# Kernel optimization log

Hardware: AMD Instinct MI355X
Metric: run time of the kernel (lower is better)

## Reference

```python
import jax, jax.numpy as jnp
import numpy as np

B, INF, OUTF, SEQ, FUT = 128, 64, 16, 512, 96
H, L = 512, 2
PROJ = INF - OUTF  # proj_size = 48 (PyTorch LSTM proj_size semantics)


def _cell(x, h, c, Wih, Whh, bih, bhh, Whr):
    # One LSTM-with-projection step; PyTorch gate order: i, f, g, o
    gates = x @ Wih.T + h @ Whh.T + bih + bhh  # (B, 4H)
    i, f, g, o = jnp.split(gates, 4, axis=-1)
    c = jax.nn.sigmoid(f) * c + jax.nn.sigmoid(i) * jnp.tanh(g)
    h = (jax.nn.sigmoid(o) * jnp.tanh(c)) @ Whr.T  # projected hidden (B, PROJ)
    return h, c


def _run_layer(xs, p):
    # xs: (T, B, F) time-major; returns (T, B, PROJ), final (h, c)
    Wih, Whh, bih, bhh, Whr = p
    bsz = xs.shape[1]
    h0 = jnp.zeros((bsz, PROJ), xs.dtype)
    c0 = jnp.zeros((bsz, H), xs.dtype)
    def step(carry, x_t):
        h, c = carry
        h, c = _cell(x_t, h, c, Wih, Whh, bih, bhh, Whr)
        return (h, c), h
    (hT, cT), hs = jax.lax.scan(step, (h0, c0), xs)
    return hs, hT, cT


def _encoder(x_btf, layers):
    xs = jnp.swapaxes(x_btf, 0, 1)  # (T, B, INF)
    hTs, cTs = [], []
    for p in layers:
        xs, hT, cT = _run_layer(xs, p)
        hTs.append(hT); cTs.append(cT)
    return jnp.swapaxes(xs, 0, 1), tuple(hTs), tuple(cTs)


def _decoder(h0s, c0s, first_prev, dec_btf, layers):
    xs = jnp.swapaxes(dec_btf, 0, 1)  # (FUT, B, OUTF)
    def step(carry, x_t):
        hs, cs, prev = carry
        inp = jnp.concatenate([prev, x_t], axis=-1)  # (B, INF)
        nh, nc = [], []
        for l, p in enumerate(layers):
            h, c = _cell(inp, hs[l], cs[l], *p)
            nh.append(h); nc.append(c)
            inp = h
        return (tuple(nh), tuple(nc), inp), inp
    _, preds = jax.lax.scan(step, (h0s, c0s, first_prev), xs)
    return jnp.swapaxes(preds, 0, 1)  # (B, FUT, PROJ)


def _forward(theta, insample_x_t, outsample_x_t, enc_layers, dec_layers):
    x = jnp.transpose(insample_x_t, (0, 2, 1))      # (B, SEQ, INF)
    dec = jnp.transpose(outsample_x_t, (0, 2, 1))   # (B, FUT, OUTF)
    backcast_seq, hTs, cTs = _encoder(x, enc_layers)  # (B, SEQ, PROJ)
    first_prev = x[:, -1, :PROJ]  # input_elements[:, -1, :-OUTF]
    preds = _decoder(hTs, cTs, first_prev, dec, dec_layers)  # (B, FUT, PROJ)
    backcast_basis = jnp.transpose(backcast_seq, (0, 2, 1))  # (B, PROJ, SEQ)
    forecast_basis = jnp.transpose(preds, (0, 2, 1))         # (B, PROJ, FUT)
    cut = forecast_basis.shape[1]
    backcast = jnp.einsum('bp,bpt->bt', theta[:, cut:], backcast_basis)
    forecast = jnp.einsum('bp,bpt->bt', theta[:, :cut], forecast_basis)
    return backcast, forecast


def setup_inputs() -> dict:
    key = jax.random.key(0)
    ks = iter(jax.random.split(key, 64))
    s = 1.0 / float(np.sqrt(H))
    def u(shape):
        return jax.random.uniform(next(ks), shape, jnp.float32, -s, s)
    inp = {
        "theta": jax.random.normal(next(ks), (B, 2 * PROJ), jnp.float32),
        "insample_x_t": jax.random.normal(next(ks), (B, INF, SEQ), jnp.float32),
        "outsample_x_t": jax.random.normal(next(ks), (B, OUTF, FUT), jnp.float32),
    }
    for net in ("enc", "dec"):
        for l in range(L):
            in_dim = INF if l == 0 else PROJ
            inp[f"{net}_Wih{l}"] = u((4 * H, in_dim))
            inp[f"{net}_Whh{l}"] = u((4 * H, PROJ))
            inp[f"{net}_bih{l}"] = u((4 * H,))
            inp[f"{net}_bhh{l}"] = u((4 * H,))
            inp[f"{net}_Whr{l}"] = u((PROJ, H))
    return inp


def reference(theta, insample_x_t, outsample_x_t,
              enc_Wih0, enc_Whh0, enc_bih0, enc_bhh0, enc_Whr0,
              enc_Wih1, enc_Whh1, enc_bih1, enc_bhh1, enc_Whr1,
              dec_Wih0, dec_Whh0, dec_bih0, dec_bhh0, dec_Whr0,
              dec_Wih1, dec_Whh1, dec_bih1, dec_bhh1, dec_Whr1):
    enc_layers = [(enc_Wih0, enc_Whh0, enc_bih0, enc_bhh0, enc_Whr0),
                  (enc_Wih1, enc_Whh1, enc_bih1, enc_bhh1, enc_Whr1)]
    dec_layers = [(dec_Wih0, dec_Whh0, dec_bih0, dec_bhh0, dec_Whr0),
                  (dec_Wih1, dec_Whh1, dec_bih1, dec_bhh1, dec_Whr1)]
    return _forward(theta, insample_x_t, outsample_x_t, enc_layers, dec_layers)
```

## Files before the change

kernel.cpp:

```cpp
#include <hip/hip_runtime.h>
#include <cstdint>
#include <cstddef>

#define BATCH 128
#define INF   64
#define OUTF  16
#define SEQ   512
#define FUT   96
#define HID   512
#define G4    2048
#define PROJ  48
#define ECH   4

#define DRG 8
#define DBG 8
#define DUP 64
#define DBP 16

typedef float f32x4 __attribute__((ext_vector_type(4)));

__device__ __forceinline__ float fsigmoid(float x) {
    float e = __builtin_amdgcn_exp2f(-1.4426950408889634f * x);
    return __builtin_amdgcn_rcpf(1.0f + e);
}
__device__ __forceinline__ float ftanh(float x) {
    float e = __builtin_amdgcn_exp2f(2.8853900817779268f * x);
    return 1.0f - 2.0f * __builtin_amdgcn_rcpf(1.0f + e);
}

__device__ __forceinline__ float gload(const float* p) {
    return __hip_atomic_load(p, __ATOMIC_RELAXED, __HIP_MEMORY_SCOPE_AGENT);
}
__device__ __forceinline__ void gstore(float* p, float v) {
    __hip_atomic_store(p, v, __ATOMIC_RELAXED, __HIP_MEMORY_SCOPE_AGENT);
}

__device__ __forceinline__ f32x4 gsum8(const float* p, size_t stride) {
    f32x4 a0, a1, a2, a3, a4, a5, a6, a7;
    asm volatile(
        "global_load_dwordx4 %0, %8, off sc0 sc1\n\t"
        "global_load_dwordx4 %1, %9, off sc0 sc1\n\t"
        "global_load_dwordx4 %2, %10, off sc0 sc1\n\t"
        "global_load_dwordx4 %3, %11, off sc0 sc1\n\t"
        "global_load_dwordx4 %4, %12, off sc0 sc1\n\t"
        "global_load_dwordx4 %5, %13, off sc0 sc1\n\t"
        "global_load_dwordx4 %6, %14, off sc0 sc1\n\t"
        "global_load_dwordx4 %7, %15, off sc0 sc1\n\t"
        "s_waitcnt vmcnt(0)"
        : "=&v"(a0), "=&v"(a1), "=&v"(a2), "=&v"(a3),
          "=&v"(a4), "=&v"(a5), "=&v"(a6), "=&v"(a7)
        : "v"(p), "v"(p + stride), "v"(p + 2 * stride), "v"(p + 3 * stride),
          "v"(p + 4 * stride), "v"(p + 5 * stride), "v"(p + 6 * stride),
          "v"(p + 7 * stride)
        : "memory");
    return ((a0 + a1) + (a2 + a3)) + ((a4 + a5) + (a6 + a7));
}

__device__ __forceinline__ void bsync(unsigned* ctr, unsigned target, int tid) {
    asm volatile("s_waitcnt vmcnt(0)" ::: "memory");
    __syncthreads();
    if (tid == 0) {
        __hip_atomic_fetch_add(ctr, 1u, __ATOMIC_RELAXED, __HIP_MEMORY_SCOPE_AGENT);
        while (__hip_atomic_load(ctr, __ATOMIC_RELAXED, __HIP_MEMORY_SCOPE_AGENT) < target)
            __builtin_amdgcn_s_sleep(2);
    }
    __syncthreads();
    asm volatile("" ::: "memory");
}

__global__ void k_wtrans(const float* __restrict__ W, float* __restrict__ WT,
                         int R, int C) {
    __shared__ float tile[32][33];
    int r0 = blockIdx.x * 32, c0 = blockIdx.y * 32;
    int tx = threadIdx.x, ty = threadIdx.y;
    #pragma unroll
    for (int i = 0; i < 4; ++i) {
        int r = r0 + ty + 8 * i;
        if (r < R && c0 + tx < C) tile[ty + 8 * i][tx] = W[(size_t)r * C + c0 + tx];
    }
    __syncthreads();
    #pragma unroll
    for (int i = 0; i < 4; ++i) {
        int c = c0 + ty + 8 * i;
        if (c < C && r0 + tx < R) WT[(size_t)c * R + r0 + tx] = tile[tx][ty + 8 * i];
    }
}

__global__ __launch_bounds__(512) void k_enc(
    const float* __restrict__ x,
    const float* __restrict__ WT0, const float* __restrict__ Whh0,
    const float* __restrict__ bih0, const float* __restrict__ bhh0,
    const float* __restrict__ Whr0,
    const float* __restrict__ WT1, const float* __restrict__ Whh1,
    const float* __restrict__ bih1, const float* __restrict__ bhh1,
    const float* __restrict__ Whr1,
    float* __restrict__ H0x, float* __restrict__ H1,
    float* __restrict__ hs, float* __restrict__ cs,
    unsigned* __restrict__ eflags)
{
    const bool L1w = blockIdx.x >= BATCH;
    const int b = L1w ? blockIdx.x - BATCH : blockIdx.x;
    const int j = threadIdx.x;
    const int wave = j >> 6, lane = j & 63;
    const float* WT  = L1w ? WT1 : WT0;
    const float* Whh = L1w ? Whh1 : Whh0;
    const float* Whr = L1w ? Whr1 : Whr0;
    const float* bih = L1w ? bih1 : bih0;
    const float* bhh = L1w ? bhh1 : bhh0;
    const int K = L1w ? PROJ : INF;

    __shared__ float whr[PROJ][HID + 4];
    __shared__ __align__(16) float xs[ECH][INF + 4];
    __shared__ __align__(16) float ht_lds[HID];
    __shared__ __align__(16) float h_cur[PROJ];

    float wI[PROJ], wF[PROJ], wG[PROJ], wO[PROJ];
    #pragma unroll
    for (int k4 = 0; k4 < 12; ++k4) {
        float4 vi = *reinterpret_cast<const float4*>(&Whh[(size_t)j * PROJ + 4 * k4]);
        float4 vf = *reinterpret_cast<const float4*>(&Whh[(size_t)(j + HID) * PROJ + 4 * k4]);
        float4 vg = *reinterpret_cast<const float4*>(&Whh[(size_t)(j + 2 * HID) * PROJ + 4 * k4]);
        float4 vo = *reinterpret_cast<const float4*>(&Whh[(size_t)(j + 3 * HID) * PROJ + 4 * k4]);
        wI[4*k4+0]=vi.x; wI[4*k4+1]=vi.y; wI[4*k4+2]=vi.z; wI[4*k4+3]=vi.w;
        wF[4*k4+0]=vf.x; wF[4*k4+1]=vf.y; wF[4*k4+2]=vf.z; wF[4*k4+3]=vf.w;
        wG[4*k4+0]=vg.x; wG[4*k4+1]=vg.y; wG[4*k4+2]=vg.z; wG[4*k4+3]=vg.w;
        wO[4*k4+0]=vo.x; wO[4*k4+1]=vo.y; wO[4*k4+2]=vo.z; wO[4*k4+3]=vo.w;
    }
    for (int idx = j; idx < PROJ * HID; idx += 512) {
        int p = idx >> 9, jj = idx & 511;
        whr[p][jj] = Whr[(size_t)p * HID + jj];
    }
    float bI = bih[j] + bhh[j];
    float bF = bih[j + HID] + bhh[j + HID];
    float bG = bih[j + 2 * HID] + bhh[j + 2 * HID];
    float bO = bih[j + 3 * HID] + bhh[j + 3 * HID];
    float c = 0.f;
    if (j < PROJ) h_cur[j] = 0.f;
    __syncthreads();

    for (int t0 = 0; t0 < SEQ; t0 += ECH) {
        if (!L1w) {
            if (j < INF * ECH) {
                int k = j >> 2, dt = j & 3;
                xs[dt][k] = x[(size_t)b * INF * SEQ + (size_t)k * SEQ + t0 + dt];
            }
        } else {
            if (j == 0) {
                unsigned need = (unsigned)(t0 / ECH) + 1;
                while (__hip_atomic_load(&eflags[b * 16], __ATOMIC_RELAXED,
                                         __HIP_MEMORY_SCOPE_AGENT) < need)
                    __builtin_amdgcn_s_sleep(2);
            }
            __syncthreads();
            asm volatile("" ::: "memory");
            if (j < PROJ * ECH) {
                int dt = j / PROJ, p = j % PROJ;
                xs[dt][p] = gload(&H0x[((size_t)(t0 + dt) * BATCH + b) * PROJ + p]);
            }
        }
        __syncthreads();

        float a0[ECH], a1[ECH], a2[ECH], a3[ECH];
        #pragma unroll
        for (int dt = 0; dt < ECH; ++dt) {
            a0[dt] = bI; a1[dt] = bF; a2[dt] = bG; a3[dt] = bO;
        }
        for (int kq = 0; kq < K / 4; ++kq) {
            float wi0 = WT[(size_t)(kq*4+0) * G4 + j];
            float wi1 = WT[(size_t)(kq*4+1) * G4 + j];
            float wi2 = WT[(size_t)(kq*4+2) * G4 + j];
            float wi3 = WT[(size_t)(kq*4+3) * G4 + j];
            float wf0 = WT[(size_t)(kq*4+0) * G4 + HID + j];
            float wf1 = WT[(size_t)(kq*4+1) * G4 + HID + j];
            float wf2 = WT[(size_t)(kq*4+2) * G4 + HID + j];
            float wf3 = WT[(size_t)(kq*4+3) * G4 + HID + j];
            float wg0 = WT[(size_t)(kq*4+0) * G4 + 2 * HID + j];
            float wg1 = WT[(size_t)(kq*4+1) * G4 + 2 * HID + j];
            float wg2 = WT[(size_t)(kq*4+2) * G4 + 2 * HID + j];
            float wg3 = WT[(size_t)(kq*4+3) * G4 + 2 * HID + j];
            float wo0 = WT[(size_t)(kq*4+0) * G4 + 3 * HID + j];
            float wo1 = WT[(size_t)(kq*4+1) * G4 + 3 * HID + j];
            float wo2 = WT[(size_t)(kq*4+2) * G4 + 3 * HID + j];
            float wo3 = WT[(size_t)(kq*4+3) * G4 + 3 * HID + j];
            #pragma unroll
            for (int dt = 0; dt < ECH; ++dt) {
                float4 xv = *reinterpret_cast<const float4*>(&xs[dt][kq * 4]);
                a0[dt] += wi0*xv.x + wi1*xv.y + wi2*xv.z + wi3*xv.w;
                a1[dt] += wf0*xv.x + wf1*xv.y + wf2*xv.z + wf3*xv.w;
                a2[dt] += wg0*xv.x + wg1*xv.y + wg2*xv.z + wg3*xv.w;
                a3[dt] += wo0*xv.x + wo1*xv.y + wo2*xv.z + wo3*xv.w;
            }
        }

        #pragma unroll
        for (int dt = 0; dt < ECH; ++dt) {
            float ai = a0[dt], af = a1[dt], ag = a2[dt], ao = a3[dt];
            #pragma unroll
            for (int k4 = 0; k4 < 12; ++k4) {
                float4 h4 = *reinterpret_cast<const float4*>(&h_cur[4 * k4]);
                ai += wI[4*k4+0]*h4.x + wI[4*k4+1]*h4.y + wI[4*k4+2]*h4.z + wI[4*k4+3]*h4.w;
                af += wF[4*k4+0]*h4.x + wF[4*k4+1]*h4.y + wF[4*k4+2]*h4.z + wF[4*k4+3]*h4.w;
                ag += wG[4*k4+0]*h4.x + wG[4*k4+1]*h4.y + wG[4*k4+2]*h4.z + wG[4*k4+3]*h4.w;
                ao += wO[4*k4+0]*h4.x + wO[4*k4+1]*h4.y + wO[4*k4+2]*h4.z + wO[4*k4+3]*h4.w;
            }
            float si = fsigmoid(ai), sf = fsigmoid(af), so = fsigmoid(ao), tg = ftanh(ag);
            c = sf * c + si * tg;
            ht_lds[j] = so * ftanh(c);
            __syncthreads();
            float rq[6];
            #pragma unroll
            for (int q = 0; q < 6; ++q) {
                int p = wave * 6 + q;
                float s = 0.f;
                #pragma unroll
                for (int m = 0; m < 8; ++m)
                    s += whr[p][lane + 64 * m] * ht_lds[lane + 64 * m];
                #pragma unroll
                for (int o = 32; o; o >>= 1) s += __shfl_xor(s, o, 64);
                rq[q] = s;
            }
            if (lane == 0) {
                int t = t0 + dt;
                #pragma unroll
                for (int q = 0; q < 6; ++q) {
                    int p = wave * 6 + q;
                    float v = rq[q];
                    h_cur[p] = v;
                    if (!L1w) gstore(&H0x[((size_t)t * BATCH + b) * PROJ + p], v);
                    else      H1[((size_t)t * BATCH + b) * PROJ + p] = v;
                }
            }
            __syncthreads();
        }
        if (!L1w) {
            asm volatile("s_waitcnt vmcnt(0)" ::: "memory");
            __syncthreads();
            if (j == 0)
                __hip_atomic_store(&eflags[b * 16], (unsigned)(t0 / ECH) + 1,
                                   __ATOMIC_RELAXED, __HIP_MEMORY_SCOPE_AGENT);
        }
    }
    cs[((size_t)(L1w ? BATCH : 0) + b) * HID + j] = c;
    if (j < PROJ) hs[((size_t)(L1w ? BATCH : 0) + b) * PROJ + j] = h_cur[j];
}

__global__ __launch_bounds__(512) void k_decP(
    const float* __restrict__ xdec,
    const float* __restrict__ Wih0, const float* __restrict__ Whh0,
    const float* __restrict__ bih0, const float* __restrict__ bhh0,
    const float* __restrict__ Whr0,
    const float* __restrict__ Wih1, const float* __restrict__ Whh1,
    const float* __restrict__ bih1, const float* __restrict__ bhh1,
    const float* __restrict__ Whr1,
    const float* __restrict__ hs, const float* __restrict__ cs,
    const float* __restrict__ xin,
    float* __restrict__ PPa, float* __restrict__ PPb,
    float* __restrict__ PRED,
    unsigned* __restrict__ bar)
{
    const int bg = blockIdx.x & 7, rg = blockIdx.x >> 3;
    const int tid = threadIdx.x;
    const int kq = tid & 3, rhalf = tid >> 2;
    const int u2 = tid >> 3, b2 = tid & 7;
    const int uglob = rg * DUP + u2;
    const int w = tid >> 6, lane = tid & 63;
    const size_t PSTR = (size_t)BATCH * PROJ;
    const size_t DPP  = (size_t)DRG * PSTR;

    __shared__ __align__(16) float inp0[DBP][120];
    __shared__ __align__(16) float h1b[DBP][52];
    __shared__ __align__(16) float h0n[DBP][52];
    __shared__ float xch[4][DUP][17];
    __shared__ float htl[DBP][68];
    __shared__ float wslT0[DUP][52];
    __shared__ float wslT1[DUP][52];

    for (int i = tid; i < PROJ * DUP; i += 512) {
        int p = i >> 6, uu = i & 63;
        wslT0[uu][p] = Whr0[(size_t)p * HID + rg * DUP + uu];
        wslT1[uu][p] = Whr1[(size_t)p * HID + rg * DUP + uu];
    }
    float bs0[4], bs1[4];
    #pragma unroll
    for (int gg = 0; gg < 4; ++gg) {
        bs0[gg] = bih0[gg * HID + uglob] + bhh0[gg * HID + uglob];
        bs1[gg] = bih1[gg * HID + uglob] + bhh1[gg * HID + uglob];
    }
    float c0[2], c1[2];
    #pragma unroll
    for (int hh = 0; hh < 2; ++hh) {
        int bglob = bg * DBP + b2 + 8 * hh;
        c0[hh] = cs[(size_t)bglob * HID + uglob];
        c1[hh] = cs[(size_t)(BATCH + bglob) * HID + uglob];
    }
    __syncthreads();

    unsigned* ctr = bar + bg * 64;
    unsigned phase = 0;

    for (int t = 0; t < FUT; ++t) {
        const float* ppaR = PPa + (size_t)((t - 1) & 1) * DPP;
        float*       ppaW = PPa + (size_t)(t & 1) * DPP;
        const float* ppbR = PPb + (size_t)((t - 1) & 1) * DPP;
        float*       ppbW = PPb + (size_t)(t & 1) * DPP;

        if (t == 0) {
            for (int i = tid; i < DBP * PROJ; i += 512) {
                int b = i / PROJ, p = i % PROJ;
                int bglob = bg * DBP + b;
                inp0[b][p]      = hs[(size_t)bglob * PROJ + p];
                inp0[b][48 + p] = xin[(size_t)bglob * INF * SEQ + (size_t)p * SEQ + (SEQ - 1)];
                h1b[b][p]       = hs[(size_t)(BATCH + bglob) * PROJ + p];
            }
            if (tid < DBP * OUTF) {
                int b = tid >> 4, f = tid & 15;
                inp0[b][96 + f] = xdec[(size_t)(bg * DBP + b) * (OUTF * FUT) + (size_t)f * FUT];
            }
        } else {
            if (tid < 192) {
                int b = tid / 12, p = (tid % 12) * 4;
                int bglob = bg * DBP + b;
                f32x4 s = gsum8(ppaR + (size_t)bglob * PROJ + p, PSTR);
                *reinterpret_cast<f32x4*>(&inp0[b][p]) = s;
            } else if (tid < 384) {
                int idx = tid - 192;
                int b = idx / 12, p = (idx % 12) * 4;
                int bglob = bg * DBP + b;
                f32x4 s = gsum8(ppbR + (size_t)bglob * PROJ + p, PSTR);
                *reinterpret_cast<f32x4*>(&inp0[b][48 + p]) = s;
                *reinterpret_cast<f32x4*>(&h1b[b][p]) = s;
                if (rg == 0)
                    *reinterpret_cast<f32x4*>(&PRED[((size_t)(t - 1) * BATCH + bglob) * PROJ + p]) = s;
            } else {
                #pragma unroll
                for (int rep = 0; rep < 2; ++rep) {
                    int i2 = (tid - 384) + rep * 128;
                    int b = i2 >> 4, f = i2 & 15;
                    inp0[b][96 + f] = xdec[(size_t)(bg * DBP + b) * (OUTF * FUT) + (size_t)f * FUT + t];
                }
            }
        }
        __syncthreads();

        #pragma unroll
        for (int p = 0; p < 2; ++p) {
            int rid = p * 128 + rhalf;
            int g = rid >> 6, u = rid & 63;
            int grow = g * HID + rg * DUP + u;
            float wv[28];
            #pragma unroll
            for (int kk = 0; kk < 28; ++kk) {
                int k = kq * 28 + kk;
                wv[kk] = (k < 48) ? Whh0[(size_t)grow * 48 + k]
                                  : Wih0[(size_t)grow * 64 + (k - 48)];
            }
            float acc[DBP];
            #pragma unroll
            for (int b = 0; b < DBP; ++b) acc[b] = 0.f;
            const float* srcA = &inp0[0][0] + kq * 28;
            #pragma unroll
            for (int i4 = 0; i4 < 7; ++i4) {
                float w0 = wv[i4*4], w1 = wv[i4*4+1], w2 = wv[i4*4+2], w3 = wv[i4*4+3];
                #pragma unroll
                for (int b = 0; b < DBP; ++b) {
                    float4 xv = *reinterpret_cast<const float4*>(&srcA[b * 120 + i4 * 4]);
                    acc[b] += w0*xv.x + w1*xv.y + w2*xv.z + w3*xv.w;
                }
            }
            #pragma unroll
            for (int b = 0; b < DBP; ++b) {
                acc[b] += __shfl_xor(acc[b], 1, 64);
                acc[b] += __shfl_xor(acc[b], 2, 64);
            }
            if (kq == 0) {
                #pragma unroll
                for (int b = 0; b < DBP; ++b) xch[g][u][b] = acc[b];
            }
        }
        __syncthreads();
        #pragma unroll
        for (int hh = 0; hh < 2; ++hh) {
            int b = b2 + 8 * hh;
            float gi = xch[0][u2][b] + bs0[0];
            float gf = xch[1][u2][b] + bs0[1];
            float gc = xch[2][u2][b] + bs0[2];
            float go = xch[3][u2][b] + bs0[3];
            float si = fsigmoid(gi), sf = fsigmoid(gf), so = fsigmoid(go), tg = ftanh(gc);
            c0[hh] = sf * c0[hh] + si * tg;
            htl[b][u2] = so * ftanh(c0[hh]);
        }
        __syncthreads();
        if (lane < PROJ) {
            #pragma unroll
            for (int bb = 0; bb < 2; ++bb) {
                int b = 2 * w + bb;
                float s = 0.f;
                #pragma unroll
                for (int u4 = 0; u4 < 16; ++u4) {
                    float4 hv = *reinterpret_cast<const float4*>(&htl[b][u4 * 4]);
                    s += wslT0[u4*4+0][lane]*hv.x + wslT0[u4*4+1][lane]*hv.y
                       + wslT0[u4*4+2][lane]*hv.z + wslT0[u4*4+3][lane]*hv.w;
                }
                gstore(&ppaW[(size_t)rg * PSTR + (size_t)(bg * DBP + b) * PROJ + lane], s);
            }
        }
        phase += 1;
        bsync(ctr, phase * DRG, tid);

        if (tid < 192) {
            int b = tid / 12, p = (tid % 12) * 4;
            f32x4 s = gsum8(ppaW + (size_t)(bg * DBP + b) * PROJ + p, PSTR);
            *reinterpret_cast<f32x4*>(&h0n[b][p]) = s;
        }
        __syncthreads();

        #pragma unroll
        for (int p = 0; p < 2; ++p) {
            int rid = p * 128 + rhalf;
            int g = rid >> 6, u = rid & 63;
            int grow = g * HID + rg * DUP + u;
            float wv[24];
            #pragma unroll
            for (int kk = 0; kk < 24; ++kk) {
                int k = kq * 24 + kk;
                wv[kk] = (k < 48) ? Whh1[(size_t)grow * 48 + k]
                                  : Wih1[(size_t)grow * 48 + (k - 48)];
            }
            const float* srcB = (kq < 2) ? (&h1b[0][0] + kq * 24)
                                         : (&h0n[0][0] + (kq - 2) * 24);
            float acc[DBP];
            #pragma unroll
            for (int b = 0; b < DBP; ++b) acc[b] = 0.f;
            #pragma unroll
            for (int i4 = 0; i4 < 6; ++i4) {
                float w0 = wv[i4*4], w1 = wv[i4*4+1], w2 = wv[i4*4+2], w3 = wv[i4*4+3];
                #pragma unroll
                for (int b = 0; b < DBP; ++b) {
                    float4 xv = *reinterpret_cast<const float4*>(&srcB[b * 52 + i4 * 4]);
                    acc[b] += w0*xv.x + w1*xv.y + w2*xv.z + w3*xv.w;
                }
            }
            #pragma unroll
            for (int b = 0; b < DBP; ++b) {
                acc[b] += __shfl_xor(acc[b], 1, 64);
                acc[b] += __shfl_xor(acc[b], 2, 64);
            }
            if (kq == 0) {
                #pragma unroll
                for (int b = 0; b < DBP; ++b) xch[g][u][b] = acc[b];
            }
        }
        __syncthreads();
        #pragma unroll
        for (int hh = 0; hh < 2; ++hh) {
            int b = b2 + 8 * hh;
            float gi = xch[0][u2][b] + bs1[0];
            float gf = xch[1][u2][b] + bs1[1];
            float gc = xch[2][u2][b] + bs1[2];
            float go = xch[3][u2][b] + bs1[3];
            float si = fsigmoid(gi), sf = fsigmoid(gf), so = fsigmoid(go), tg = ftanh(gc);
            c1[hh] = sf * c1[hh] + si * tg;
            htl[b][u2] = so * ftanh(c1[hh]);
        }
        __syncthreads();
        if (lane < PROJ) {
            #pragma unroll
            for (int bb = 0; bb < 2; ++bb) {
                int b = 2 * w + bb;
                float s = 0.f;
                #pragma unroll
                for (int u4 = 0; u4 < 16; ++u4) {
                    float4 hv = *reinterpret_cast<const float4*>(&htl[b][u4 * 4]);
                    s += wslT1[u4*4+0][lane]*hv.x + wslT1[u4*4+1][lane]*hv.y
                       + wslT1[u4*4+2][lane]*hv.z + wslT1[u4*4+3][lane]*hv.w;
                }
                gstore(&ppbW[(size_t)rg * PSTR + (size_t)(bg * DBP + b) * PROJ + lane], s);
            }
        }
        phase += 1;
        bsync(ctr, phase * DRG, tid);
    }

    if (tid < 2 * PROJ) {
        int bb = tid / PROJ, p = tid % PROJ;
        int bglob = bg * DBP + 2 * rg + bb;
        const float* ppbF = PPb + (size_t)((FUT - 1) & 1) * DPP;
        float s = 0.f;
        #pragma unroll
        for (int rr = 0; rr < DRG; ++rr)
            s += gload(&ppbF[(size_t)rr * PSTR + (size_t)bglob * PROJ + p]);
        PRED[((size_t)(FUT - 1) * BATCH + bglob) * PROJ + p] = s;
    }
}

__global__ void k_final(const float* __restrict__ theta, const float* __restrict__ H1,
                        const float* __restrict__ PRED, float* __restrict__ out)
{
    int b = blockIdx.x;
    __shared__ float th[2 * PROJ];
    if (threadIdx.x < 2 * PROJ) th[threadIdx.x] = theta[(size_t)b * 2 * PROJ + threadIdx.x];
    __syncthreads();
    for (int t = threadIdx.x; t < SEQ; t += 256) {
        float s = 0.f;
        #pragma unroll
        for (int p = 0; p < PROJ; ++p) s += th[PROJ + p] * H1[((size_t)t * BATCH + b) * PROJ + p];
        out[(size_t)b * SEQ + t] = s;
    }
    for (int t = threadIdx.x; t < FUT; t += 256) {
        float s = 0.f;
        #pragma unroll
        for (int p = 0; p < PROJ; ++p) s += th[p] * PRED[((size_t)t * BATCH + b) * PROJ + p];
        out[(size_t)BATCH * SEQ + (size_t)b * FUT + t] = s;
    }
}

extern "C" void kernel_launch(void* const* d_in, const int* in_sizes, int n_in,
                              void* d_out, int out_size, void* d_ws, size_t ws_size,
                              hipStream_t stream)
{
    (void)in_sizes; (void)n_in; (void)out_size; (void)ws_size;
    const float* theta = (const float*)d_in[0];
    const float* xin   = (const float*)d_in[1];
    const float* xdec  = (const float*)d_in[2];
    const float* eW0i = (const float*)d_in[3];
    const float* eW0h = (const float*)d_in[4];
    const float* eb0i = (const float*)d_in[5];
    const float* eb0h = (const float*)d_in[6];
    const float* eW0r = (const float*)d_in[7];
    const float* eW1i = (const float*)d_in[8];
    const float* eW1h = (const float*)d_in[9];
    const float* eb1i = (const float*)d_in[10];
    const float* eb1h = (const float*)d_in[11];
    const float* eW1r = (const float*)d_in[12];
    const float* dW0i = (const float*)d_in[13];
    const float* dW0h = (const float*)d_in[14];
    const float* db0i = (const float*)d_in[15];
    const float* db0h = (const float*)d_in[16];
    const float* dW0r = (const float*)d_in[17];
    const float* dW1i = (const float*)d_in[18];
    const float* dW1h = (const float*)d_in[19];
    const float* db1i = (const float*)d_in[20];
    const float* db1h = (const float*)d_in[21];
    const float* dW1r = (const float*)d_in[22];

    float* ws = (float*)d_ws;
    size_t off = 0;
    float* H0x  = ws + off; off += (size_t)SEQ * BATCH * PROJ;
    float* H1   = ws + off; off += (size_t)SEQ * BATCH * PROJ;
    float* PRED = ws + off; off += (size_t)FUT * BATCH * PROJ;
    float* hs   = ws + off; off += (size_t)2 * BATCH * PROJ;
    float* cs   = ws + off; off += (size_t)2 * BATCH * HID;
    float* WT0  = ws + off; off += (size_t)INF * G4;
    float* WT1  = ws + off; off += (size_t)PROJ * G4;
    const size_t DPP = (size_t)DRG * BATCH * PROJ;
    float* PPa  = ws + off; off += 2 * DPP;
    float* PPb  = ws + off; off += 2 * DPP;
    off = (off + 63) & ~(size_t)63;
    unsigned* eflags = (unsigned*)(ws + off); off += BATCH * 16;
    unsigned* bar    = (unsigned*)(ws + off); off += DBG * 64;

    hipMemsetAsync(eflags, 0, (BATCH * 16 + DBG * 64) * sizeof(unsigned), stream);
    k_wtrans<<<dim3(G4 / 32, 2), dim3(32, 8), 0, stream>>>(eW0i, WT0, G4, INF);
    k_wtrans<<<dim3(G4 / 32, 2), dim3(32, 8), 0, stream>>>(eW1i, WT1, G4, PROJ);
    k_enc<<<2 * BATCH, 512, 0, stream>>>(xin,
                                         WT0, eW0h, eb0i, eb0h, eW0r,
                                         WT1, eW1h, eb1i, eb1h, eW1r,
                                         H0x, H1, hs, cs, eflags);
    k_decP<<<DRG * DBG, 512, 0, stream>>>(xdec, dW0i, dW0h, db0i, db0h, dW0r,
                                          dW1i, dW1h, db1i, db1h, dW1r,
                                          hs, cs, xin, PPa, PPb, PRED, bar);
    k_final<<<BATCH, 256, 0, stream>>>(theta, H1, PRED, (float*)d_out);
}
```

Before: 5.507 ms.

## Split encoder gate rows across 1024 threads to halve per-thread register weights

The encoder block grows from 512 to 1024 threads. Each half holds two of the four gate rows of the recurrent weights in registers instead of all four. The upper half writes its g/o preactivations to LDS, and the lower half computes the cell update after an extra barrier. The projection reduction is spread over 16 waves with 3 outputs each. This is meant to cut register pressure and add parallelism per timestep, at the cost of one more __syncthreads per step and LDS traffic for the gate exchange.

```diff
diff --git a/kernel.cpp b/kernel.cpp
--- a/kernel.cpp
+++ b/kernel.cpp
@@ -86,7 +86,7 @@
     }
 }
 
-__global__ __launch_bounds__(512) void k_enc(
+__global__ __launch_bounds__(1024) void k_enc(
     const float* __restrict__ x,
     const float* __restrict__ WT0, const float* __restrict__ Whh0,
     const float* __restrict__ bih0, const float* __restrict__ bhh0,
@@ -100,8 +100,10 @@
 {
     const bool L1w = blockIdx.x >= BATCH;
     const int b = L1w ? blockIdx.x - BATCH : blockIdx.x;
-    const int j = threadIdx.x;
-    const int wave = j >> 6, lane = j & 63;
+    const int tid = threadIdx.x;
+    const int j = tid & 511;
+    const int half = tid >> 9;
+    const int wave = tid >> 6, lane = tid & 63;
     const float* WT  = L1w ? WT1 : WT0;
     const float* Whh = L1w ? Whh1 : Whh0;
     const float* Whr = L1w ? Whr1 : Whr0;
@@ -113,39 +115,38 @@
     __shared__ __align__(16) float xs[ECH][INF + 4];
     __shared__ __align__(16) float ht_lds[HID];
     __shared__ __align__(16) float h_cur[PROJ];
-
-    float wI[PROJ], wF[PROJ], wG[PROJ], wO[PROJ];
+    __shared__ __align__(16) float gG[HID];
+    __shared__ __align__(16) float gO[HID];
+
+    const int row0 = half ? (j + 2 * HID) : j;
+    const int row1 = half ? (j + 3 * HID) : (j + HID);
+
+    float wA[PROJ], wB[PROJ];
     #pragma unroll
     for (int k4 = 0; k4 < 12; ++k4) {
-        float4 vi = *reinterpret_cast<const float4*>(&Whh[(size_t)j * PROJ + 4 * k4]);
-        float4 vf = *reinterpret_cast<const float4*>(&Whh[(size_t)(j + HID) * PROJ + 4 * k4]);
-        float4 vg = *reinterpret_cast<const float4*>(&Whh[(size_t)(j + 2 * HID) * PROJ + 4 * k4]);
-        float4 vo = *reinterpret_cast<const float4*>(&Whh[(size_t)(j + 3 * HID) * PROJ + 4 * k4]);
-        wI[4*k4+0]=vi.x; wI[4*k4+1]=vi.y; wI[4*k4+2]=vi.z; wI[4*k4+3]=vi.w;
-        wF[4*k4+0]=vf.x; wF[4*k4+1]=vf.y; wF[4*k4+2]=vf.z; wF[4*k4+3]=vf.w;
-        wG[4*k4+0]=vg.x; wG[4*k4+1]=vg.y; wG[4*k4+2]=vg.z; wG[4*k4+3]=vg.w;
-        wO[4*k4+0]=vo.x; wO[4*k4+1]=vo.y; wO[4*k4+2]=vo.z; wO[4*k4+3]=vo.w;
-    }
-    for (int idx = j; idx < PROJ * HID; idx += 512) {
+        float4 va = *reinterpret_cast<const float4*>(&Whh[(size_t)row0 * PROJ + 4 * k4]);
+        float4 vb = *reinterpret_cast<const float4*>(&Whh[(size_t)row1 * PROJ + 4 * k4]);
+        wA[4*k4+0]=va.x; wA[4*k4+1]=va.y; wA[4*k4+2]=va.z; wA[4*k4+3]=va.w;
+        wB[4*k4+0]=vb.x; wB[4*k4+1]=vb.y; wB[4*k4+2]=vb.z; wB[4*k4+3]=vb.w;
+    }
+    for (int idx = tid; idx < PROJ * HID; idx += 1024) {
         int p = idx >> 9, jj = idx & 511;
         whr[p][jj] = Whr[(size_t)p * HID + jj];
     }
-    float bI = bih[j] + bhh[j];
-    float bF = bih[j + HID] + bhh[j + HID];
-    float bG = bih[j + 2 * HID] + bhh[j + 2 * HID];
-    float bO = bih[j + 3 * HID] + bhh[j + 3 * HID];
+    float bA = bih[row0] + bhh[row0];
+    float bB = bih[row1] + bhh[row1];
     float c = 0.f;
-    if (j < PROJ) h_cur[j] = 0.f;
+    if (tid < PROJ) h_cur[tid] = 0.f;
     __syncthreads();
 
     for (int t0 = 0; t0 < SEQ; t0 += ECH) {
         if (!L1w) {
-            if (j < INF * ECH) {
-                int k = j >> 2, dt = j & 3;
+            if (tid < INF * ECH) {
+                int k = tid >> 2, dt = tid & 3;
                 xs[dt][k] = x[(size_t)b * INF * SEQ + (size_t)k * SEQ + t0 + dt];
             }
         } else {
-            if (j == 0) {
+            if (tid == 0) {
                 unsigned need = (unsigned)(t0 / ECH) + 1;
                 while (__hip_atomic_load(&eflags[b * 16], __ATOMIC_RELAXED,
                                          __HIP_MEMORY_SCOPE_AGENT) < need)
@@ -153,64 +154,55 @@
             }
             __syncthreads();
             asm volatile("" ::: "memory");
-            if (j < PROJ * ECH) {
-                int dt = j / PROJ, p = j % PROJ;
+            if (tid < PROJ * ECH) {
+                int dt = tid / PROJ, p = tid % PROJ;
                 xs[dt][p] = gload(&H0x[((size_t)(t0 + dt) * BATCH + b) * PROJ + p]);
             }
         }
         __syncthreads();
 
-        float a0[ECH], a1[ECH], a2[ECH], a3[ECH];
-        #pragma unroll
-        for (int dt = 0; dt < ECH; ++dt) {
-            a0[dt] = bI; a1[dt] = bF; a2[dt] = bG; a3[dt] = bO;
-        }
+        float aA[ECH], aB[ECH];
+        #pragma unroll
+        for (int dt = 0; dt < ECH; ++dt) { aA[dt] = bA; aB[dt] = bB; }
         for (int kq = 0; kq < K / 4; ++kq) {
-            float wi0 = WT[(size_t)(kq*4+0) * G4 + j];
-            float wi1 = WT[(size_t)(kq*4+1) * G4 + j];
-            float wi2 = WT[(size_t)(kq*4+2) * G4 + j];
-            float wi3 = WT[(size_t)(kq*4+3) * G4 + j];
-            float wf0 = WT[(size_t)(kq*4+0) * G4 + HID + j];
-            float wf1 = WT[(size_t)(kq*4+1) * G4 + HID + j];
-            float wf2 = WT[(size_t)(kq*4+2) * G4 + HID + j];
-            float wf3 = WT[(size_t)(kq*4+3) * G4 + HID + j];
-            float wg0 = WT[(size_t)(kq*4+0) * G4 + 2 * HID + j];
-            float wg1 = WT[(size_t)(kq*4+1) * G4 + 2 * HID + j];
-            float wg2 = WT[(size_t)(kq*4+2) * G4 + 2 * HID + j];
-            float wg3 = WT[(size_t)(kq*4+3) * G4 + 2 * HID + j];
-            float wo0 = WT[(size_t)(kq*4+0) * G4 + 3 * HID + j];
-            float wo1 = WT[(size_t)(kq*4+1) * G4 + 3 * HID + j];
-            float wo2 = WT[(size_t)(kq*4+2) * G4 + 3 * HID + j];
-            float wo3 = WT[(size_t)(kq*4+3) * G4 + 3 * HID + j];
+            float wa0 = WT[(size_t)(kq*4+0) * G4 + row0];
+            float wa1 = WT[(size_t)(kq*4+1) * G4 + row0];
+            float wa2 = WT[(size_t)(kq*4+2) * G4 + row0];
+            float wa3 = WT[(size_t)(kq*4+3) * G4 + row0];
+            float wb0 = WT[(size_t)(kq*4+0) * G4 + row1];
+            float wb1 = WT[(size_t)(kq*4+1) * G4 + row1];
+            float wb2 = WT[(size_t)(kq*4+2) * G4 + row1];
+            float wb3 = WT[(size_t)(kq*4+3) * G4 + row1];
             #pragma unroll
             for (int dt = 0; dt < ECH; ++dt) {
                 float4 xv = *reinterpret_cast<const float4*>(&xs[dt][kq * 4]);
-                a0[dt] += wi0*xv.x + wi1*xv.y + wi2*xv.z + wi3*xv.w;
-                a1[dt] += wf0*xv.x + wf1*xv.y + wf2*xv.z + wf3*xv.w;
-                a2[dt] += wg0*xv.x + wg1*xv.y + wg2*xv.z + wg3*xv.w;
-                a3[dt] += wo0*xv.x + wo1*xv.y + wo2*xv.z + wo3*xv.w;
+                aA[dt] += wa0*xv.x + wa1*xv.y + wa2*xv.z + wa3*xv.w;
+                aB[dt] += wb0*xv.x + wb1*xv.y + wb2*xv.z + wb3*xv.w;
             }
         }
 
         #pragma unroll
         for (int dt = 0; dt < ECH; ++dt) {
-            float ai = a0[dt], af = a1[dt], ag = a2[dt], ao = a3[dt];
+            float sA = aA[dt], sB = aB[dt];
             #pragma unroll
             for (int k4 = 0; k4 < 12; ++k4) {
                 float4 h4 = *reinterpret_cast<const float4*>(&h_cur[4 * k4]);
-                ai += wI[4*k4+0]*h4.x + wI[4*k4+1]*h4.y + wI[4*k4+2]*h4.z + wI[4*k4+3]*h4.w;
-                af += wF[4*k4+0]*h4.x + wF[4*k4+1]*h4.y + wF[4*k4+2]*h4.z + wF[4*k4+3]*h4.w;
-                ag += wG[4*k4+0]*h4.x + wG[4*k4+1]*h4.y + wG[4*k4+2]*h4.z + wG[4*k4+3]*h4.w;
-                ao += wO[4*k4+0]*h4.x + wO[4*k4+1]*h4.y + wO[4*k4+2]*h4.z + wO[4*k4+3]*h4.w;
-            }
-            float si = fsigmoid(ai), sf = fsigmoid(af), so = fsigmoid(ao), tg = ftanh(ag);
-            c = sf * c + si * tg;
-            ht_lds[j] = so * ftanh(c);
+                sA += wA[4*k4+0]*h4.x + wA[4*k4+1]*h4.y + wA[4*k4+2]*h4.z + wA[4*k4+3]*h4.w;
+                sB += wB[4*k4+0]*h4.x + wB[4*k4+1]*h4.y + wB[4*k4+2]*h4.z + wB[4*k4+3]*h4.w;
+            }
+            if (half) { gG[j] = sA; gO[j] = sB; }
             __syncthreads();
-            float rq[6];
-            #pragma unroll
-            for (int q = 0; q < 6; ++q) {
-                int p = wave * 6 + q;
+            if (!half) {
+                float si = fsigmoid(sA), sf = fsigmoid(sB);
+                float tg = ftanh(gG[j]), so = fsigmoid(gO[j]);
+                c = sf * c + si * tg;
+                ht_lds[j] = so * ftanh(c);
+            }
+            __syncthreads();
+            float rq[3];
+            #pragma unroll
+            for (int q = 0; q < 3; ++q) {
+                int p = wave * 3 + q;
                 float s = 0.f;
                 #pragma unroll
                 for (int m = 0; m < 8; ++m)
@@ -222,8 +214,8 @@
             if (lane == 0) {
                 int t = t0 + dt;
                 #pragma unroll
-                for (int q = 0; q < 6; ++q) {
-                    int p = wave * 6 + q;
+                for (int q = 0; q < 3; ++q) {
+                    int p = wave * 3 + q;
                     float v = rq[q];
                     h_cur[p] = v;
                     if (!L1w) gstore(&H0x[((size_t)t * BATCH + b) * PROJ + p], v);
@@ -235,13 +227,13 @@
         if (!L1w) {
             asm volatile("s_waitcnt vmcnt(0)" ::: "memory");
             __syncthreads();
-            if (j == 0)
+            if (tid == 0)
                 __hip_atomic_store(&eflags[b * 16], (unsigned)(t0 / ECH) + 1,
                                    __ATOMIC_RELAXED, __HIP_MEMORY_SCOPE_AGENT);
         }
     }
-    cs[((size_t)(L1w ? BATCH : 0) + b) * HID + j] = c;
-    if (j < PROJ) hs[((size_t)(L1w ? BATCH : 0) + b) * PROJ + j] = h_cur[j];
+    if (!half) cs[((size_t)(L1w ? BATCH : 0) + b) * HID + j] = c;
+    if (tid < PROJ) hs[((size_t)(L1w ? BATCH : 0) + b) * PROJ + tid] = h_cur[tid];
 }
 
 __global__ __launch_bounds__(512) void k_decP(
@@ -562,10 +554,10 @@
     hipMemsetAsync(eflags, 0, (BATCH * 16 + DBG * 64) * sizeof(unsigned), stream);
     k_wtrans<<<dim3(G4 / 32, 2), dim3(32, 8), 0, stream>>>(eW0i, WT0, G4, INF);
     k_wtrans<<<dim3(G4 / 32, 2), dim3(32, 8), 0, stream>>>(eW1i, WT1, G4, PROJ);
-    k_enc<<<2 * BATCH, 512, 0, stream>>>(xin,
-                                         WT0, eW0h, eb0i, eb0h, eW0r,
-                                         WT1, eW1h, eb1i, eb1h, eW1r,
-                                         H0x, H1, hs, cs, eflags);
+    k_enc<<<2 * BATCH, 1024, 0, stream>>>(xin,
+                                          WT0, eW0h, eb0i, eb0h, eW0r,
+                                          WT1, eW1h, eb1i, eb1h, eW1r,
+                                          H0x, H1, hs, cs, eflags);
     k_decP<<<DRG * DBG, 512, 0, stream>>>(xdec, dW0i, dW0h, db0i, db0h, dW0r,
                                           dW1i, dW1h, db1i, db1h, dW1r,
                                           hs, cs, xin, PPa, PPb, PRED, bar);
```

Measured after the change: 5.380 ms. 2.3% less time.
